# Kernel optimization log

Measured on AMD Instinct MI355X. Metric: run time of the kernel, lower is better.

## Reference

```python
import jax, jax.numpy as jnp
import numpy as np

EPS_NORM = 1e-12  # F.normalize eps
EPS_LOG = 1e-10
COMMITMENT_COST = 0.25


def setup_inputs() -> dict:
    key = jax.random.key(0)
    k1, k2 = jax.random.split(key)
    x = jax.random.normal(k1, (32, 256, 32, 32), dtype=jnp.float32)
    # nn.Embedding weight init: uniform(-1, 1)
    W = jax.random.uniform(k2, (1024, 256), dtype=jnp.float32, minval=-1.0, maxval=1.0)
    return {"x": x, "W": W, "n": 2}


def reference(x, W, n):
    sg = jax.lax.stop_gradient
    # NCHW -> NHWC
    inputs = jnp.transpose(x, (0, 2, 3, 1))
    B, H, Wd, D = inputs.shape
    K = W.shape[0]
    flat = inputs.reshape(-1, D)                       # [N, D]
    N = flat.shape[0]
    # squared euclidean distances via matmul: [N, K]
    distances = (jnp.sum(flat * flat, axis=1, keepdims=True)
                 + jnp.sum(W * W, axis=1)
                 - 2.0 * jnp.matmul(flat, W.T))
    # topk of -distances -> n smallest distances
    neg_vals, encoding_indices = jax.lax.top_k(-distances, n)  # [N, n]
    inv_dist = 1.0 / (-neg_vals)                        # 1/distance, [N, n]
    norm = jnp.maximum(jnp.sqrt(jnp.sum(inv_dist * inv_dist, axis=-1, keepdims=True)), EPS_NORM)
    weights = sg(inv_dist / norm)                       # detached in torch
    # scatter weights into one-hot-ish encodings [N, K]
    rows = jnp.arange(N)[:, None]
    encodings = jnp.zeros((N, K), dtype=flat.dtype).at[rows, encoding_indices].set(weights)
    quantized = jnp.matmul(encodings, W).reshape(B, H, Wd, D)
    e_latent_loss = jnp.mean((sg(quantized) - inputs) ** 2)
    q_latent_loss = jnp.mean((quantized - sg(inputs)) ** 2)
    loss = q_latent_loss + COMMITMENT_COST * e_latent_loss
    # straight-through
    quantized_st = inputs + sg(quantized - inputs)
    avg_probs = jnp.mean(encodings, axis=0)
    perplexity = jnp.exp(-jnp.sum(avg_probs * jnp.log(avg_probs + EPS_LOG)))
    return loss, jnp.transpose(quantized_st, (0, 3, 1, 2)), perplexity, encodings
```

## Files before the change

kernel.cpp:

```cpp
#include <hip/hip_runtime.h>
#include <math.h>

#define NROWS 32768
#define DIMS  256
#define KCODES 1024

typedef __attribute__((ext_vector_type(8))) short short8;
typedef __attribute__((ext_vector_type(4))) float f32x4;

static const size_t OFF_WB     = 8388608;
static const size_t OFF_WNORM  = OFF_WB + 131072;
static const size_t OFF_ENCSUM = OFF_WNORM + 1024;
static const size_t OFF_LOSSP  = OFF_ENCSUM + 1024;
static const size_t OFF_WND    = OFF_LOSSP + 8192;

static const size_t OUT_Q    = 1;
static const size_t OUT_PERP = 8388609;
static const size_t OUT_ENC  = 8388610;

__device__ inline unsigned short f2bf(float f) {
    unsigned int u = __float_as_uint(f);
    unsigned int r = u + 0x7FFFu + ((u >> 16) & 1u);
    return (unsigned short)(r >> 16);
}

__device__ inline float packdi(float d, int code) {
    return __uint_as_float((__float_as_uint(d) & 0xFFFFFC00u) | (unsigned)code);
}

__device__ __forceinline__ void gl_lds16(const void* gsrc, void* ldst) {
    typedef const __attribute__((address_space(1))) unsigned int GU;
    typedef __attribute__((address_space(3))) unsigned int LU;
    __builtin_amdgcn_global_load_lds((GU*)gsrc, (LU*)ldst, 16, 0, 0);
}

__global__ __launch_bounds__(256) void wprep(const float* __restrict__ Wm,
                                             unsigned short* __restrict__ Wb,
                                             float* __restrict__ wnorm,
                                             double* __restrict__ wnormd,
                                             float* __restrict__ enc_sum)
{
    const int r = blockIdx.x * 4 + (threadIdx.x >> 6);
    const int lane = threadIdx.x & 63;
    float4 v = ((const float4*)(Wm + (size_t)r * 256))[lane];
    ushort4 o;
    o.x = f2bf(v.x); o.y = f2bf(v.y); o.z = f2bf(v.z); o.w = f2bf(v.w);
    const int d0 = lane * 4;
    const int kk = d0 >> 5, quad = (d0 >> 3) & 3, jb = d0 & 7;
    const int tt = r >> 4, col = r & 15;
    const size_t idx = (size_t)tt * 4096 + (size_t)((kk * 4 + quad) * 16 + col) * 8 + jb;
    *(ushort4*)(Wb + idx) = o;
    double s = (double)v.x*(double)v.x + (double)v.y*(double)v.y
             + (double)v.z*(double)v.z + (double)v.w*(double)v.w;
    #pragma unroll
    for (int off = 32; off > 0; off >>= 1) s += __shfl_down(s, off);
    if (lane == 0) { wnormd[r] = s; wnorm[r] = (float)s; }
    if (blockIdx.x == 0) {
        #pragma unroll
        for (int q = 0; q < 4; ++q) enc_sum[threadIdx.x * 4 + q] = 0.0f;
    }
}

__global__ __launch_bounds__(256, 4) void gemm_topk_quant(
    const float* __restrict__ x, const unsigned short* __restrict__ Wb,
    const float* __restrict__ wnorm, const double* __restrict__ wnd,
    const float* __restrict__ Wm,
    float* __restrict__ enc_sum,
    float* __restrict__ enc,
    float* __restrict__ outq, float* __restrict__ loss_part)
{
    __shared__ __align__(16) char lds[32768];
    float*  sCd   = (float*)lds;
    int*    mIdx  = (int*)(lds + 13312);
    double* rd    = (double*)(lds + 14336);
    float*  qtile = (float*)lds;
    double* rnr   = (double*)(lds + 16896);
    int*    s0    = (int*)(lds + 17152);
    int*    s1    = (int*)(lds + 17280);
    float*  sw0   = (float*)(lds + 17408);
    float*  sw1   = (float*)(lds + 17536);
    double* sredd = (double*)(lds + 17664);
    unsigned short* xtile = (unsigned short*)(lds + 16384);

    const int t    = threadIdx.x;
    const int wave = t >> 6;
    const int g    = wave & 1;
    const int h    = wave >> 1;
    const int lane = t & 63;
    const int col  = lane & 15;
    const int quad = lane >> 4;
    const int r0   = blockIdx.x * 32;
    const int b    = r0 >> 10;
    const int hw0  = r0 & 1023;
    const float* xblk = x + (size_t)b * 262144 + hw0;

    const int row = t >> 3;
    const int q8  = t & 7;

    const char* wb_bytes = (const char*)Wb;
    {
        const char* src = wb_bytes + (size_t)(h * 32) * 8192 + g * 4096;
        char* dstl = lds + h * 8192 + g * 4096;
        #pragma unroll
        for (int q = 0; q < 4; ++q)
            gl_lds16(src + q * 1024 + lane * 16, dstl + q * 1024);
    }

    float xs[32];
    {
        const float* xr = xblk + row;
        #pragma unroll
        for (int p2 = 0; p2 < 2; ++p2)
            #pragma unroll
            for (int j = 0; j < 16; ++j)
                xs[p2 * 16 + j] = xr[(size_t)(p2 * 128 + q8 * 16 + j) * 1024];
    }

    #pragma unroll
    for (int p2 = 0; p2 < 2; ++p2)
        #pragma unroll
        for (int j4 = 0; j4 < 4; ++j4) {
            ushort4 o;
            o.x = f2bf(xs[p2 * 16 + j4 * 4 + 0]);
            o.y = f2bf(xs[p2 * 16 + j4 * 4 + 1]);
            o.z = f2bf(xs[p2 * 16 + j4 * 4 + 2]);
            o.w = f2bf(xs[p2 * 16 + j4 * 4 + 3]);
            const int xi = (row * 256 + p2 * 128 + q8 * 16 + j4 * 4) ^ ((row & 7) << 3);
            *(ushort4*)(xtile + xi) = o;
        }
    __syncthreads();

    short8 af[8];
    #pragma unroll
    for (int kk = 0; kk < 8; ++kk) {
        const int xi = ((g * 16 + col) * 256 + kk * 32 + quad * 8) ^ ((col & 7) << 3);
        af[kk] = *(const short8*)(xtile + xi);
    }
    __syncthreads();

    float m0[4], m1[4], m2[4];
    #pragma unroll
    for (int r = 0; r < 4; ++r) { m0[r] = 3.4e38f; m1[r] = 3.4e38f; m2[r] = 3.4e38f; }

    for (int cc = 0; cc < 32; ++cc) {
        if (cc < 31) {
            const char* src = wb_bytes + (size_t)(h * 32 + cc + 1) * 8192 + g * 4096;
            char* dstl = lds + ((cc + 1) & 1) * 16384 + h * 8192 + g * 4096;
            #pragma unroll
            for (int q = 0; q < 4; ++q)
                gl_lds16(src + q * 1024 + lane * 16, dstl + q * 1024);
        }
        const char* bb = lds + (cc & 1) * 16384 + h * 8192;
        f32x4 acc = {0.f, 0.f, 0.f, 0.f};
        #pragma unroll
        for (int kk = 0; kk < 8; ++kk) {
            short8 b0 = *(const short8*)(bb + kk * 1024 + lane * 16);
            acc = __builtin_amdgcn_mfma_f32_16x16x32_bf16(af[kk], b0, acc, 0, 0, 0);
        }
        const int code0 = h * 512 + cc * 16 + col;
        const float wn0 = wnorm[code0];
        #pragma unroll
        for (int r = 0; r < 4; ++r) {
            float pv0 = packdi(fmaf(-2.0f, acc[r], wn0), code0);
            float t0  = fmaxf(m0[r], pv0); m0[r] = fminf(m0[r], pv0);
            float t1  = fmaxf(m1[r], t0);  m1[r] = fminf(m1[r], t0);
            m2[r] = fminf(m2[r], t1);
        }
        __syncthreads();
    }

    #pragma unroll
    for (int r = 0; r < 4; ++r) {
        const int rl = g * 16 + quad * 4 + r;
        const int s  = h * 48 + col * 3;
        sCd[(s + 0) * 34 + rl] = m0[r];
        sCd[(s + 1) * 34 + rl] = m1[r];
        sCd[(s + 2) * 34 + rl] = m2[r];
    }
    __syncthreads();

    {
        float a0 = 3.4e38f, a1 = 3.4e38f, a2 = 3.4e38f, a3 = 3.4e38f,
              a4 = 3.4e38f, a5 = 3.4e38f, a6 = 3.4e38f, a7 = 3.4e38f;
        #pragma unroll
        for (int i = 0; i < 12; ++i) {
            float d = sCd[(q8 * 12 + i) * 34 + row];
            if (d < a7) {
                a7 = d; float tf;
                if (a7 < a6) { tf = a7; a7 = a6; a6 = tf; }
                if (a6 < a5) { tf = a6; a6 = a5; a5 = tf; }
                if (a5 < a4) { tf = a5; a5 = a4; a4 = tf; }
                if (a4 < a3) { tf = a4; a4 = a3; a3 = tf; }
                if (a3 < a2) { tf = a3; a3 = a2; a2 = tf; }
                if (a2 < a1) { tf = a2; a2 = a1; a1 = tf; }
                if (a1 < a0) { tf = a1; a1 = a0; a0 = tf; }
            }
        }
        float sel = 3.4e38f;
        #pragma unroll
        for (int q = 0; q < 8; ++q) {
            float m = a0;
            m = fminf(m, __shfl_xor(m, 1));
            m = fminf(m, __shfl_xor(m, 2));
            m = fminf(m, __shfl_xor(m, 4));
            if (q8 == q) sel = m;
            if (a0 == m) { a0 = a1; a1 = a2; a2 = a3; a3 = a4;
                           a4 = a5; a5 = a6; a6 = a7; a7 = 3.4e38f; }
        }
        mIdx[row * 8 + q8] = (int)(__float_as_uint(sel) & 1023u);
    }
    __syncthreads();

    {
        int cd[8];
        #pragma unroll
        for (int c8 = 0; c8 < 8; ++c8) cd[c8] = mIdx[row * 8 + c8];
        double dot[8];
        #pragma unroll
        for (int c8 = 0; c8 < 8; ++c8) dot[c8] = 0.0;
        double rn = 0.0;
        #pragma unroll
        for (int v = 0; v < 8; ++v) {
            const int d0 = (v >> 2) * 128 + q8 * 16 + (v & 3) * 4;
            const double x0 = (double)xs[v * 4 + 0];
            const double x1 = (double)xs[v * 4 + 1];
            const double x2 = (double)xs[v * 4 + 2];
            const double x3 = (double)xs[v * 4 + 3];
            rn += x0*x0 + x1*x1 + x2*x2 + x3*x3;
            #pragma unroll
            for (int c8 = 0; c8 < 8; ++c8) {
                const float4 wv = *(const float4*)(Wm + (size_t)cd[c8] * 256 + d0);
                dot[c8] += x0 * (double)wv.x + x1 * (double)wv.y
                         + x2 * (double)wv.z + x3 * (double)wv.w;
            }
        }
        #pragma unroll
        for (int m = 1; m < 8; m <<= 1) {
            #pragma unroll
            for (int c8 = 0; c8 < 8; ++c8) dot[c8] += __shfl_xor(dot[c8], m);
            rn += __shfl_xor(rn, m);
        }
        int myc = 0; double mydot = 0.0;
        #pragma unroll
        for (int c8 = 0; c8 < 8; ++c8)
            if (q8 == c8) { myc = cd[c8]; mydot = dot[c8]; }
        rd[row * 8 + q8] = wnd[myc] - 2.0 * mydot;
        if (q8 == 0) rnr[row] = rn;
    }
    __syncthreads();

    if (t < 32) {
        double rn = rnr[t];
        double d0 = 1e300, d1 = 1e300; int b0 = 1 << 30, b1 = 1 << 30;
        #pragma unroll
        for (int q = 0; q < 8; ++q) {
            double d = rd[t * 8 + q];
            int    c = mIdx[t * 8 + q];
            if (d < d0 || (d == d0 && c < b0)) { d1 = d0; b1 = b0; d0 = d; b0 = c; }
            else if (d < d1 || (d == d1 && c < b1)) { d1 = d; b1 = c; }
        }
        double D0 = rn + d0;
        double D1 = rn + d1;
        double inv0 = 1.0 / D0, inv1 = 1.0 / D1;
        double nrm = sqrt(inv0 * inv0 + inv1 * inv1);
        if (nrm < 1e-12) nrm = 1e-12;
        float w0 = (float)(inv0 / nrm);
        float w1 = (float)(inv1 / nrm);
        s0[t] = b0; s1[t] = b1; sw0[t] = w0; sw1[t] = w1;
        atomicAdd(&enc_sum[b0], w0);
        atomicAdd(&enc_sum[b1], w1);
    }
    __syncthreads();

    #pragma unroll
    for (int rr = 0; rr < 8; ++rr) {
        const int rw = wave * 8 + rr;
        const int i0 = s0[rw], i1 = s1[rw];
        const float w0 = sw0[rw], w1 = sw1[rw];
        f32x4* dst = (f32x4*)(enc + (size_t)(r0 + rw) * KCODES);
        #pragma unroll
        for (int it = 0; it < 4; ++it) {
            const int base = it * 256 + lane * 4;
            f32x4 v;
            v.x = (base + 0 == i0) ? w0 : ((base + 0 == i1) ? w1 : 0.0f);
            v.y = (base + 1 == i0) ? w0 : ((base + 1 == i1) ? w1 : 0.0f);
            v.z = (base + 2 == i0) ? w0 : ((base + 2 == i1) ? w1 : 0.0f);
            v.w = (base + 3 == i0) ? w0 : ((base + 3 == i1) ? w1 : 0.0f);
            dst[it * 64 + lane] = v;
        }
    }

    double ls = 0.0;
    #pragma unroll
    for (int p2 = 0; p2 < 2; ++p2) {
        const int   cA = s0[row], cB = s1[row];
        const float w0 = sw0[row], w1 = sw1[row];
        const float* W0 = Wm + (size_t)cA * 256 + p2 * 128 + q8 * 16;
        const float* W1 = Wm + (size_t)cB * 256 + p2 * 128 + q8 * 16;
        #pragma unroll
        for (int v4 = 0; v4 < 4; ++v4) {
            const float4 a  = *(const float4*)(W0 + v4 * 4);
            const float4 bv = *(const float4*)(W1 + v4 * 4);
            f32x4 qv;
            qv.x = w0 * a.x + w1 * bv.x;
            qv.y = w0 * a.y + w1 * bv.y;
            qv.z = w0 * a.z + w1 * bv.z;
            qv.w = w0 * a.w + w1 * bv.w;
            float e0 = qv.x - xs[p2 * 16 + v4 * 4 + 0];
            float e1 = qv.y - xs[p2 * 16 + v4 * 4 + 1];
            float e2 = qv.z - xs[p2 * 16 + v4 * 4 + 2];
            float e3 = qv.w - xs[p2 * 16 + v4 * 4 + 3];
            ls += (double)(e0*e0 + e1*e1 + e2*e2 + e3*e3);
            const int dl = q8 * 16 + v4 * 4;
            *(f32x4*)(qtile + row * 132 + dl) = qv;
        }
        __syncthreads();
        #pragma unroll
        for (int p = 0; p < 4; ++p) {
            const int task = p * 256 + t;
            const int cl   = task >> 3;
            const int hwq  = task & 7;
            f32x4 v;
            v.x = qtile[(hwq * 4 + 0) * 132 + cl];
            v.y = qtile[(hwq * 4 + 1) * 132 + cl];
            v.z = qtile[(hwq * 4 + 2) * 132 + cl];
            v.w = qtile[(hwq * 4 + 3) * 132 + cl];
            *(f32x4*)(outq + ((size_t)(b * 256 + p2 * 128 + cl)) * 1024 + hw0 + hwq * 4) = v;
        }
        __syncthreads();
    }

    #pragma unroll
    for (int off = 32; off > 0; off >>= 1) ls += __shfl_down(ls, off);
    if (lane == 0) sredd[wave] = ls;
    __syncthreads();
    if (t == 0) {
        double s = 0.0;
        #pragma unroll
        for (int w = 0; w < 4; ++w) s += sredd[w];
        loss_part[blockIdx.x] = (float)s;
    }
}

__global__ __launch_bounds__(256) void finalize_k(const float* __restrict__ enc_sum,
                                                  const float* __restrict__ loss_part,
                                                  float* __restrict__ out)
{
    __shared__ double sh[256];
    const int t = threadIdx.x;
    double ls = 0.0;
    for (int i = t; i < 1024; i += 256) ls += (double)loss_part[i];
    sh[t] = ls; __syncthreads();
    for (int s = 128; s > 0; s >>= 1) { if (t < s) sh[t] += sh[t + s]; __syncthreads(); }
    double loss_sum = sh[0];
    __syncthreads();
    double ps = 0.0;
    for (int k = t; k < KCODES; k += 256) {
        double p = (double)enc_sum[k] / (double)NROWS;
        ps += p * log(p + 1e-10);
    }
    sh[t] = ps; __syncthreads();
    for (int s = 128; s > 0; s >>= 1) { if (t < s) sh[t] += sh[t + s]; __syncthreads(); }
    if (t == 0) {
        out[0]        = (float)(1.25 * loss_sum / 8388608.0);
        out[OUT_PERP] = (float)exp(-sh[0]);
    }
}

extern "C" void kernel_launch(void* const* d_in, const int* in_sizes, int n_in,
                              void* d_out, int out_size, void* d_ws, size_t ws_size,
                              hipStream_t stream)
{
    const float* x  = (const float*)d_in[0];
    const float* Wm = (const float*)d_in[1];
    float* out = (float*)d_out;
    float* ws  = (float*)d_ws;

    unsigned short* Wb      = (unsigned short*)(ws + OFF_WB);
    float*          wnorm   = ws + OFF_WNORM;
    float*          enc_sum = ws + OFF_ENCSUM;
    float*          loss_p  = ws + OFF_LOSSP;
    double*         wnd     = (double*)(ws + OFF_WND);

    wprep<<<KCODES / 4, 256, 0, stream>>>(Wm, Wb, wnorm, wnd, enc_sum);
    gemm_topk_quant<<<NROWS / 32, 256, 0, stream>>>(x, Wb, wnorm, wnd, Wm, enc_sum,
                                                    out + OUT_ENC, out + OUT_Q, loss_p);
    finalize_k<<<1, 256, 0, stream>>>(enc_sum, loss_p, out);
}
```

Baseline: 261.0 us.

## Triple-buffer codebook tiles with fine-grained vmcnt waits and stage wnorm in LDS

```diff
diff --git a/kernel.cpp b/kernel.cpp
--- a/kernel.cpp
+++ b/kernel.cpp
@@ -61,7 +61,7 @@
     }
 }
 
-__global__ __launch_bounds__(256, 4) void gemm_topk_quant(
+__global__ __launch_bounds__(256, 3) void gemm_topk_quant(
     const float* __restrict__ x, const unsigned short* __restrict__ Wb,
     const float* __restrict__ wnorm, const double* __restrict__ wnd,
     const float* __restrict__ Wm,
@@ -69,7 +69,7 @@
     float* __restrict__ enc,
     float* __restrict__ outq, float* __restrict__ loss_part)
 {
-    __shared__ __align__(16) char lds[32768];
+    __shared__ __align__(16) char lds[53248];
     float*  sCd   = (float*)lds;
     int*    mIdx  = (int*)(lds + 13312);
     double* rd    = (double*)(lds + 14336);
@@ -80,7 +80,8 @@
     float*  sw0   = (float*)(lds + 17408);
     float*  sw1   = (float*)(lds + 17536);
     double* sredd = (double*)(lds + 17664);
-    unsigned short* xtile = (unsigned short*)(lds + 16384);
+    unsigned short* xtile = (unsigned short*)(lds + 32768);
+    float*  wnLds = (float*)(lds + 49152);
 
     const int t    = threadIdx.x;
     const int wave = t >> 6;
@@ -97,15 +98,6 @@
     const int row = t >> 3;
     const int q8  = t & 7;
 
-    const char* wb_bytes = (const char*)Wb;
-    {
-        const char* src = wb_bytes + (size_t)(h * 32) * 8192 + g * 4096;
-        char* dstl = lds + h * 8192 + g * 4096;
-        #pragma unroll
-        for (int q = 0; q < 4; ++q)
-            gl_lds16(src + q * 1024 + lane * 16, dstl + q * 1024);
-    }
-
     float xs[32];
     {
         const float* xr = xblk + row;
@@ -114,6 +106,21 @@
             #pragma unroll
             for (int j = 0; j < 16; ++j)
                 xs[p2 * 16 + j] = xr[(size_t)(p2 * 128 + q8 * 16 + j) * 1024];
+    }
+
+    const char* wb_bytes = (const char*)Wb;
+    {
+        const char* s0p = wb_bytes + (size_t)(h * 32 + 0) * 8192 + g * 4096;
+        const char* s1p = wb_bytes + (size_t)(h * 32 + 1) * 8192 + g * 4096;
+        char* d0p = lds + 0 * 16384 + h * 8192 + g * 4096;
+        char* d1p = lds + 1 * 16384 + h * 8192 + g * 4096;
+        #pragma unroll
+        for (int q = 0; q < 4; ++q) {
+            gl_lds16(s0p + q * 1024 + lane * 16, d0p + q * 1024);
+            gl_lds16(s1p + q * 1024 + lane * 16, d1p + q * 1024);
+        }
+        gl_lds16((const char*)wnorm + wave * 1024 + lane * 16,
+                 (char*)wnLds + wave * 1024);
     }
 
     #pragma unroll
@@ -142,15 +149,17 @@
     #pragma unroll
     for (int r = 0; r < 4; ++r) { m0[r] = 3.4e38f; m1[r] = 3.4e38f; m2[r] = 3.4e38f; }
 
+    int bi = 0;
+    int bj = 2;
     for (int cc = 0; cc < 32; ++cc) {
-        if (cc < 31) {
-            const char* src = wb_bytes + (size_t)(h * 32 + cc + 1) * 8192 + g * 4096;
-            char* dstl = lds + ((cc + 1) & 1) * 16384 + h * 8192 + g * 4096;
+        if (cc < 30) {
+            const char* src = wb_bytes + (size_t)(h * 32 + cc + 2) * 8192 + g * 4096;
+            char* dstl = lds + bj * 16384 + h * 8192 + g * 4096;
             #pragma unroll
             for (int q = 0; q < 4; ++q)
                 gl_lds16(src + q * 1024 + lane * 16, dstl + q * 1024);
         }
-        const char* bb = lds + (cc & 1) * 16384 + h * 8192;
+        const char* bb = lds + bi * 16384 + h * 8192;
         f32x4 acc = {0.f, 0.f, 0.f, 0.f};
         #pragma unroll
         for (int kk = 0; kk < 8; ++kk) {
@@ -158,7 +167,7 @@
             acc = __builtin_amdgcn_mfma_f32_16x16x32_bf16(af[kk], b0, acc, 0, 0, 0);
         }
         const int code0 = h * 512 + cc * 16 + col;
-        const float wn0 = wnorm[code0];
+        const float wn0 = wnLds[code0];
         #pragma unroll
         for (int r = 0; r < 4; ++r) {
             float pv0 = packdi(fmaf(-2.0f, acc[r], wn0), code0);
@@ -166,7 +175,16 @@
             float t1  = fmaxf(m1[r], t0);  m1[r] = fminf(m1[r], t0);
             m2[r] = fminf(m2[r], t1);
         }
-        __syncthreads();
+        __builtin_amdgcn_sched_barrier(0);
+        if (cc < 30) {
+            asm volatile("s_waitcnt vmcnt(4)" ::: "memory");
+        } else if (cc == 30) {
+            asm volatile("s_waitcnt vmcnt(0)" ::: "memory");
+        }
+        __builtin_amdgcn_s_barrier();
+        __builtin_amdgcn_sched_barrier(0);
+        bi = (bi == 2) ? 0 : bi + 1;
+        bj = (bj == 2) ? 0 : bj + 1;
     }
 
     #pragma unroll
```

Result: no change. 261.1 us (+0.0%).

## Overlap encodings zero-fill with GEMM loop and scatter top-2 weights

Applied to the files above, without the earlier changes.

```diff
diff --git a/kernel.cpp b/kernel.cpp
--- a/kernel.cpp
+++ b/kernel.cpp
@@ -69,7 +69,7 @@
     float* __restrict__ enc,
     float* __restrict__ outq, float* __restrict__ loss_part)
 {
-    __shared__ __align__(16) char lds[32768];
+    __shared__ __align__(16) char lds[36864];
     float*  sCd   = (float*)lds;
     int*    mIdx  = (int*)(lds + 13312);
     double* rd    = (double*)(lds + 14336);
@@ -81,6 +81,7 @@
     float*  sw1   = (float*)(lds + 17536);
     double* sredd = (double*)(lds + 17664);
     unsigned short* xtile = (unsigned short*)(lds + 16384);
+    float*  wnLds = (float*)(lds + 32768);
 
     const int t    = threadIdx.x;
     const int wave = t >> 6;
@@ -104,6 +105,8 @@
         #pragma unroll
         for (int q = 0; q < 4; ++q)
             gl_lds16(src + q * 1024 + lane * 16, dstl + q * 1024);
+        gl_lds16((const char*)wnorm + wave * 1024 + lane * 16,
+                 (char*)wnLds + wave * 1024);
     }
 
     float xs[32];
@@ -142,6 +145,7 @@
     #pragma unroll
     for (int r = 0; r < 4; ++r) { m0[r] = 3.4e38f; m1[r] = 3.4e38f; m2[r] = 3.4e38f; }
 
+    const f32x4 zero4 = {0.f, 0.f, 0.f, 0.f};
     for (int cc = 0; cc < 32; ++cc) {
         if (cc < 31) {
             const char* src = wb_bytes + (size_t)(h * 32 + cc + 1) * 8192 + g * 4096;
@@ -150,21 +154,26 @@
             for (int q = 0; q < 4; ++q)
                 gl_lds16(src + q * 1024 + lane * 16, dstl + q * 1024);
         }
+        *(f32x4*)(enc + (size_t)(r0 + cc) * KCODES + t * 4) = zero4;
+
         const char* bb = lds + (cc & 1) * 16384 + h * 8192;
-        f32x4 acc = {0.f, 0.f, 0.f, 0.f};
-        #pragma unroll
-        for (int kk = 0; kk < 8; ++kk) {
+        f32x4 acc_a = {0.f, 0.f, 0.f, 0.f};
+        f32x4 acc_b = {0.f, 0.f, 0.f, 0.f};
+        #pragma unroll
+        for (int kk = 0; kk < 4; ++kk) {
             short8 b0 = *(const short8*)(bb + kk * 1024 + lane * 16);
-            acc = __builtin_amdgcn_mfma_f32_16x16x32_bf16(af[kk], b0, acc, 0, 0, 0);
+            short8 b1 = *(const short8*)(bb + (kk + 4) * 1024 + lane * 16);
+            acc_a = __builtin_amdgcn_mfma_f32_16x16x32_bf16(af[kk], b0, acc_a, 0, 0, 0);
+            acc_b = __builtin_amdgcn_mfma_f32_16x16x32_bf16(af[kk + 4], b1, acc_b, 0, 0, 0);
         }
         const int code0 = h * 512 + cc * 16 + col;
-        const float wn0 = wnorm[code0];
+        const float wn0 = wnLds[code0];
         #pragma unroll
         for (int r = 0; r < 4; ++r) {
-            float pv0 = packdi(fmaf(-2.0f, acc[r], wn0), code0);
-            float t0  = fmaxf(m0[r], pv0); m0[r] = fminf(m0[r], pv0);
-            float t1  = fmaxf(m1[r], t0);  m1[r] = fminf(m1[r], t0);
-            m2[r] = fminf(m2[r], t1);
+            float pv0 = packdi(fmaf(-2.0f, acc_a[r] + acc_b[r], wn0), code0);
+            m2[r] = __builtin_amdgcn_fmed3f(m1[r], m2[r], pv0);
+            m1[r] = __builtin_amdgcn_fmed3f(m0[r], m1[r], pv0);
+            m0[r] = fminf(m0[r], pv0);
         }
         __syncthreads();
     }
@@ -269,26 +278,10 @@
         s0[t] = b0; s1[t] = b1; sw0[t] = w0; sw1[t] = w1;
         atomicAdd(&enc_sum[b0], w0);
         atomicAdd(&enc_sum[b1], w1);
-    }
-    __syncthreads();
-
-    #pragma unroll
-    for (int rr = 0; rr < 8; ++rr) {
-        const int rw = wave * 8 + rr;
-        const int i0 = s0[rw], i1 = s1[rw];
-        const float w0 = sw0[rw], w1 = sw1[rw];
-        f32x4* dst = (f32x4*)(enc + (size_t)(r0 + rw) * KCODES);
-        #pragma unroll
-        for (int it = 0; it < 4; ++it) {
-            const int base = it * 256 + lane * 4;
-            f32x4 v;
-            v.x = (base + 0 == i0) ? w0 : ((base + 0 == i1) ? w1 : 0.0f);
-            v.y = (base + 1 == i0) ? w0 : ((base + 1 == i1) ? w1 : 0.0f);
-            v.z = (base + 2 == i0) ? w0 : ((base + 2 == i1) ? w1 : 0.0f);
-            v.w = (base + 3 == i0) ? w0 : ((base + 3 == i1) ? w1 : 0.0f);
-            dst[it * 64 + lane] = v;
-        }
-    }
+        enc[(size_t)(r0 + t) * KCODES + b0] = w0;
+        enc[(size_t)(r0 + t) * KCODES + b1] = w1;
+    }
+    __syncthreads();
 
     double ls = 0.0;
     #pragma unroll
```

After: 253.7 us. 2.8% less time.
